# Optimization experiments

Measured on AMD Instinct MI355X. Metric: run time of the kernel, lower is better.

Reference implementation:

```python
import jax, jax.numpy as jnp
import numpy as np

VOCAB = 50257
D_MODEL = 768
N_LAYERS = 4
N_HEADS = 12
D_HEAD = D_MODEL // N_HEADS
MAX_LEN = 5000
EPS = 1e-5


def _make_pe(max_len, d_model):
    # sinusoidal PE, interleaved sin/cos, base n=10000 (matches PositionalEncodingLayer)
    pos = jnp.arange(max_len, dtype=jnp.float32)[:, None]            # [L,1]
    i = jnp.arange(d_model // 2, dtype=jnp.float32)[None, :]         # [1,D/2]
    theta = pos / jnp.power(10000.0, 2.0 * i / d_model)              # [L,D/2]
    pe = jnp.zeros((max_len, d_model), dtype=jnp.float32)
    pe = pe.at[:, 0::2].set(jnp.sin(theta))
    pe = pe.at[:, 1::2].set(jnp.cos(theta))
    return pe


def setup_inputs() -> dict:
    key = jax.random.key(0)
    ks = jax.random.split(key, 10)
    B, S = 2, 1024
    tokens = jax.random.randint(ks[0], (B, S), 0, VOCAB)
    std = 0.02
    embed = jax.random.normal(ks[1], (VOCAB, D_MODEL), jnp.float32) * std
    pe = _make_pe(MAX_LEN, D_MODEL)
    # per-layer stacked params, torch nn.Linear convention: y = x @ W.T + b
    wq_w = jax.random.normal(ks[2], (N_LAYERS, D_MODEL, D_MODEL), jnp.float32) * std
    wk_w = jax.random.normal(ks[3], (N_LAYERS, D_MODEL, D_MODEL), jnp.float32) * std
    wv_w = jax.random.normal(ks[4], (N_LAYERS, D_MODEL, D_MODEL), jnp.float32) * std
    lin_w = jax.random.normal(ks[5], (N_LAYERS, D_MODEL, D_MODEL), jnp.float32) * std
    wq_b = jnp.zeros((N_LAYERS, D_MODEL), jnp.float32)
    wk_b = jnp.zeros((N_LAYERS, D_MODEL), jnp.float32)
    wv_b = jnp.zeros((N_LAYERS, D_MODEL), jnp.float32)
    lin_b = jnp.zeros((N_LAYERS, D_MODEL), jnp.float32)
    n1_s = jnp.ones((N_LAYERS, D_MODEL), jnp.float32)
    n1_b = jnp.zeros((N_LAYERS, D_MODEL), jnp.float32)
    n2_s = jnp.ones((N_LAYERS, D_MODEL), jnp.float32)
    n2_b = jnp.zeros((N_LAYERS, D_MODEL), jnp.float32)
    unembed_w = jax.random.normal(ks[6], (VOCAB, D_MODEL), jnp.float32) * std
    unembed_b = jnp.zeros((VOCAB,), jnp.float32)
    return dict(tokens=tokens, embed=embed, pe=pe,
                wq_w=wq_w, wq_b=wq_b, wk_w=wk_w, wk_b=wk_b, wv_w=wv_w, wv_b=wv_b,
                lin_w=lin_w, lin_b=lin_b, n1_s=n1_s, n1_b=n1_b, n2_s=n2_s, n2_b=n2_b,
                unembed_w=unembed_w, unembed_b=unembed_b)


def _layernorm(x, scale, bias):
    m = jnp.mean(x, axis=-1, keepdims=True)
    v = jnp.mean(jnp.square(x - m), axis=-1, keepdims=True)
    return (x - m) * jax.lax.rsqrt(v + EPS) * scale + bias


def _attn_block(x, wq_w, wq_b, wk_w, wk_b, wv_w, wv_b, lin_w, lin_b, n1_s, n1_b, n2_s, n2_b):
    B, S, D = x.shape
    def proj(w, b):
        y = x @ w.T + b
        return y.reshape(B, S, N_HEADS, D_HEAD).transpose(0, 2, 1, 3)  # [B,H,S,Dh]
    q, k, v = proj(wq_w, wq_b), proj(wk_w, wk_b), proj(wv_w, wv_b)
    scores = jnp.einsum('bhqd,bhkd->bhqk', q, k) / jnp.sqrt(jnp.float32(D_HEAD))
    causal = jnp.tril(jnp.ones((S, S), dtype=bool))
    scores = jnp.where(causal, scores, -jnp.inf)
    probs = jax.nn.softmax(scores, axis=-1)
    attn = jnp.einsum('bhqk,bhkd->bhqd', probs, v)
    attn = attn.transpose(0, 2, 1, 3).reshape(B, S, D)
    x = _layernorm(x + attn, n1_s, n1_b)
    x = _layernorm(x + (x @ lin_w.T + lin_b), n2_s, n2_b)
    return x


def reference(tokens, embed, pe, wq_w, wq_b, wk_w, wk_b, wv_w, wv_b,
              lin_w, lin_b, n1_s, n1_b, n2_s, n2_b, unembed_w, unembed_b):
    B, S = tokens.shape
    x = embed[tokens] + pe[:S]
    for l in range(N_LAYERS):
        x = _attn_block(x, wq_w[l], wq_b[l], wk_w[l], wk_b[l], wv_w[l], wv_b[l],
                        lin_w[l], lin_b[l], n1_s[l], n1_b[l], n2_s[l], n2_b[l])
    logits = x @ unembed_w.T + unembed_b
    return logits
```

## Files before the change

kernel.cpp:

```cpp
#include <hip/hip_runtime.h>
#include <hip/hip_bf16.h>


#define VOCAB 50257
#define DM 768
#define NL 4
#define NH 12
#define DH 64
#define SEQ 1024
#define BATCH 2
#define ROWS (BATCH * SEQ)
#define QKVN (3 * DM)

typedef __attribute__((ext_vector_type(8))) short short8;
typedef __attribute__((ext_vector_type(4))) float f32x4;

__device__ __forceinline__ unsigned short f2bf(float f) {
    union { float f; unsigned u; } v; v.f = f;
    unsigned r = v.u + 0x7FFFu + ((v.u >> 16) & 1u);
    return (unsigned short)(r >> 16);
}

#define GLOAD16(gp, lp)                                                        \
    __builtin_amdgcn_global_load_lds(                                          \
        (const __attribute__((address_space(1))) unsigned int*)(gp),           \
        (__attribute__((address_space(3))) unsigned int*)(lp), 16, 0, 0)

__global__ __launch_bounds__(256) void cvt_kernel(const float* __restrict__ in,
                                                  unsigned short* __restrict__ out,
                                                  int n4) {
    int i = blockIdx.x * 256 + threadIdx.x;
    if (i < n4) {
        float4 v = ((const float4*)in)[i];
        ushort4 o;
        o.x = f2bf(v.x); o.y = f2bf(v.y); o.z = f2bf(v.z); o.w = f2bf(v.w);
        ((ushort4*)out)[i] = o;
    }
}

__global__ __launch_bounds__(256) void cvt_qkv_kernel(const float* __restrict__ wq,
                                                      const float* __restrict__ wk,
                                                      const float* __restrict__ wv,
                                                      unsigned short* __restrict__ dst,
                                                      int n4) {
    int i = blockIdx.x * 256 + threadIdx.x;
    if (i >= n4) return;
    const int PER_L = 3 * DM * DM / 4, PER_W = DM * DM / 4;
    int l = i / PER_L;
    int rem = i - l * PER_L;
    int w = rem / PER_W;
    int r2 = rem - w * PER_W;
    const float* src = (w == 0) ? wq : (w == 1) ? wk : wv;
    float4 v = ((const float4*)src)[(size_t)l * PER_W + r2];
    ushort4 o;
    o.x = f2bf(v.x); o.y = f2bf(v.y); o.z = f2bf(v.z); o.w = f2bf(v.w);
    ((ushort4*)dst)[i] = o;
}

__global__ __launch_bounds__(256) void pack_qkv_bias(const float* __restrict__ bq,
                                                     const float* __restrict__ bk,
                                                     const float* __restrict__ bv,
                                                     float* __restrict__ dst) {
    int i = blockIdx.x * 256 + threadIdx.x;
    if (i >= NL * QKVN) return;
    int l = i / QKVN, c = i - l * QKVN;
    int w = c / DM, cc = c - w * DM;
    const float* src = (w == 0) ? bq : (w == 1) ? bk : bv;
    dst[i] = src[l * DM + cc];
}

__global__ __launch_bounds__(256) void embed_kernel(const int* __restrict__ tok,
                                                    const float* __restrict__ emb,
                                                    const float* __restrict__ pe,
                                                    float* __restrict__ xf,
                                                    unsigned short* __restrict__ xb) {
    int row = blockIdx.x;
    int t = tok[row];
    int s = row & (SEQ - 1);
    #pragma unroll
    for (int j = 0; j < 3; ++j) {
        int c = threadIdx.x + j * 256;
        float v = emb[(size_t)t * DM + c] + pe[(size_t)s * DM + c];
        xf[(size_t)row * DM + c] = v;
        xb[(size_t)row * DM + c] = f2bf(v);
    }
}

__device__ __forceinline__ float block_sum(float x, float* red) {
    #pragma unroll
    for (int off = 32; off > 0; off >>= 1) x += __shfl_down(x, off);
    int w = threadIdx.x >> 6;
    if ((threadIdx.x & 63) == 0) red[w] = x;
    __syncthreads();
    float t = (red[0] + red[1]) + (red[2] + red[3]);
    __syncthreads();
    return t;
}

__global__ __launch_bounds__(256) void ln_kernel(const float* __restrict__ A,
                                                 const float* __restrict__ Bi,
                                                 const float* __restrict__ sc,
                                                 const float* __restrict__ bi,
                                                 float* __restrict__ xf,
                                                 unsigned short* __restrict__ xb) {
    __shared__ float red[4];
    int row = blockIdx.x, tid = threadIdx.x;
    const float* ap = A + (size_t)row * DM;
    const float* bp = Bi + (size_t)row * DM;
    float v[3], sum = 0.f;
    #pragma unroll
    for (int j = 0; j < 3; ++j) { v[j] = ap[tid + j * 256] + bp[tid + j * 256]; sum += v[j]; }
    sum = block_sum(sum, red);
    float mean = sum * (1.f / DM);
    float vs = 0.f;
    #pragma unroll
    for (int j = 0; j < 3; ++j) { float d = v[j] - mean; vs += d * d; }
    vs = block_sum(vs, red);
    float rstd = rsqrtf(vs * (1.f / DM) + 1e-5f);
    #pragma unroll
    for (int j = 0; j < 3; ++j) {
        int c = tid + j * 256;
        float o = (v[j] - mean) * rstd * sc[c] + bi[c];
        xf[(size_t)row * DM + c] = o;
        xb[(size_t)row * DM + c] = f2bf(o);
    }
}

template <int OUT_BF16>
__global__ __launch_bounds__(256) void gemm128(const unsigned short* __restrict__ A,
                                               const unsigned short* __restrict__ B,
                                               const float* __restrict__ bias,
                                               void* __restrict__ C,
                                               int M, int N, int K, int gx) {
    __shared__ __align__(16) unsigned short As[128 * 64];
    __shared__ __align__(16) unsigned short Bs[128 * 64];
    int bid = blockIdx.x;
    const int nwg = gridDim.x;
    if ((nwg & 7) == 0) {
        int q = nwg >> 3;
        bid = (bid & 7) * q + (bid >> 3);
    }
    const int bx = bid % gx, by = bid / gx;
    const int m0 = bx * 128, n0 = by * 128;
    const int tid = threadIdx.x, lane = tid & 63, wid = tid >> 6;
    const int wm = wid >> 1, wn = wid & 1;
    const int lr = lane & 15, lq = lane >> 4;

    const int sr = wid * 32 + (lane >> 3);
    const int sch = lane & 7;
    const int scs = sch ^ (sr & 7);
    const unsigned short* aP[4];
    const unsigned short* bP[4];
    unsigned short* aL[4];
    unsigned short* bL[4];
    #pragma unroll
    for (int i = 0; i < 4; ++i) {
        int r = sr + i * 8;
        aP[i] = A + (size_t)(m0 + r) * K + scs * 8;
        int br = n0 + r; if (br >= N) br = N - 1;
        bP[i] = B + (size_t)br * K + scs * 8;
        aL[i] = &As[r * 64 + sch * 8];
        bL[i] = &Bs[r * 64 + sch * 8];
    }

    f32x4 acc[4][4] = {};

    for (int k0 = 0; k0 < K; k0 += 64) {
        #pragma unroll
        for (int i = 0; i < 4; ++i) GLOAD16(aP[i] + k0, aL[i]);
        #pragma unroll
        for (int i = 0; i < 4; ++i) GLOAD16(bP[i] + k0, bL[i]);
        __syncthreads();
        #pragma unroll
        for (int kk = 0; kk < 2; ++kk) {
            short8 a[4], b[4];
            #pragma unroll
            for (int i = 0; i < 4; ++i) {
                int ar = wm * 64 + i * 16 + lr;
                a[i] = *reinterpret_cast<const short8*>(
                    &As[ar * 64 + (((kk * 4 + lq) ^ (ar & 7)) * 8)]);
                int br = wn * 64 + i * 16 + lr;
                b[i] = *reinterpret_cast<const short8*>(
                    &Bs[br * 64 + (((kk * 4 + lq) ^ (br & 7)) * 8)]);
            }
            #pragma unroll
            for (int i = 0; i < 4; ++i)
                #pragma unroll
                for (int j = 0; j < 4; ++j)
                    acc[i][j] = __builtin_amdgcn_mfma_f32_16x16x32_bf16(a[i], b[j], acc[i][j], 0, 0, 0);
        }
        __syncthreads();
    }
    #pragma unroll
    for (int i = 0; i < 4; ++i) {
        int row = m0 + wm * 64 + i * 16 + lq * 4;
        #pragma unroll
        for (int j = 0; j < 4; ++j) {
            int col = n0 + wn * 64 + j * 16 + lr;
            if (col < N) {
                float bv = bias[col];
                #pragma unroll
                for (int r = 0; r < 4; ++r) {
                    float v = acc[i][j][r] + bv;
                    if (OUT_BF16) ((unsigned short*)C)[(size_t)(row + r) * N + col] = f2bf(v);
                    else          ((float*)C)[(size_t)(row + r) * N + col] = v;
                }
            }
        }
    }
}

__global__ __launch_bounds__(256) void attn_kernel(const unsigned short* __restrict__ Q,
                                                   const unsigned short* __restrict__ K,
                                                   const unsigned short* __restrict__ V,
                                                   int ld,
                                                   float* __restrict__ O) {
    __shared__ __align__(16) unsigned short Ks[64 * 64];
    __shared__ __align__(16) unsigned short Vs[64 * 64];
    __shared__ __align__(16) unsigned short Ps[4][16 * 64];
    const int qb = blockIdx.x;
    const int bh = blockIdx.y;
    const int b = bh / NH, h = bh % NH;
    const int tid = threadIdx.x, lane = tid & 63, w = tid >> 6;
    const int lr = lane & 15, lq = lane >> 4;
    const int wq0 = qb * 64 + w * 16;
    const size_t base = (size_t)b * SEQ * ld + h * DH;
    const size_t obase = (size_t)b * SEQ * DM + h * DH;

    short8 qf[2];
    {
        const unsigned short* qp = Q + base + (size_t)(wq0 + lr) * ld + lq * 8;
        qf[0] = *reinterpret_cast<const short8*>(qp);
        qf[1] = *reinterpret_cast<const short8*>(qp + 32);
    }
    f32x4 o_acc[4] = {};
    float mrow[4], lrow[4];
    #pragma unroll
    for (int r = 0; r < 4; ++r) { mrow[r] = -1e30f; lrow[r] = 0.f; }

    const int srow = tid >> 3, scol = (tid & 7) * 8;
    for (int t = 0; t <= qb; ++t) {
        const int kv0 = t * 64;
        #pragma unroll
        for (int rr = 0; rr < 2; ++rr) {
            int row = rr * 32 + srow;
            {
                const unsigned short* kp = K + base + (size_t)(kv0 + row) * ld + scol;
                short8 v = *reinterpret_cast<const short8*>(kp);
                *reinterpret_cast<short8*>(&Ks[(row * 64 + scol) ^ ((row & 7) << 3)]) = v;
            }
            {
                const unsigned short* vp = V + base + (size_t)(kv0 + row) * ld + scol;
                short8 v = *reinterpret_cast<const short8*>(vp);
                #pragma unroll
                for (int j = 0; j < 8; ++j) {
                    int d = scol + j;
                    Vs[(d * 64 + row) ^ ((d & 7) << 3)] = (unsigned short)v[j];
                }
            }
        }
        __syncthreads();
        if (kv0 <= wq0 + 15) {
            f32x4 s[4];
            #pragma unroll
            for (int n = 0; n < 4; ++n) {
                int br = n * 16 + lr;
                short8 b0 = *reinterpret_cast<const short8*>(&Ks[(br * 64 + lq * 8) ^ ((br & 7) << 3)]);
                short8 b1 = *reinterpret_cast<const short8*>(&Ks[(br * 64 + 32 + lq * 8) ^ ((br & 7) << 3)]);
                f32x4 z = {};
                z = __builtin_amdgcn_mfma_f32_16x16x32_bf16(qf[0], b0, z, 0, 0, 0);
                z = __builtin_amdgcn_mfma_f32_16x16x32_bf16(qf[1], b1, z, 0, 0, 0);
                s[n] = z;
            }
            const bool diag = (t == qb);
            #pragma unroll
            for (int n = 0; n < 4; ++n)
                #pragma unroll
                for (int r = 0; r < 4; ++r) {
                    float v = s[n][r] * 0.125f;
                    if (diag) {
                        int rg = wq0 + lq * 4 + r;
                        int cg = kv0 + n * 16 + lr;
                        if (cg > rg) v = -1e30f;
                    }
                    s[n][r] = v;
                }
            float f[4];
            #pragma unroll
            for (int r = 0; r < 4; ++r) {
                float mx = fmaxf(fmaxf(s[0][r], s[1][r]), fmaxf(s[2][r], s[3][r]));
                #pragma unroll
                for (int off = 1; off < 16; off <<= 1) mx = fmaxf(mx, __shfl_xor(mx, off));
                float mn = fmaxf(mrow[r], mx);
                f[r] = exp2f((mrow[r] - mn) * 1.44269504f);
                mrow[r] = mn;
            }
            #pragma unroll
            for (int n = 0; n < 4; ++n)
                #pragma unroll
                for (int r = 0; r < 4; ++r)
                    s[n][r] = exp2f((s[n][r] - mrow[r]) * 1.44269504f);
            #pragma unroll
            for (int r = 0; r < 4; ++r) {
                float ls = ((s[0][r] + s[1][r]) + (s[2][r] + s[3][r]));
                #pragma unroll
                for (int off = 1; off < 16; off <<= 1) ls += __shfl_xor(ls, off);
                lrow[r] = lrow[r] * f[r] + ls;
            }
            #pragma unroll
            for (int n = 0; n < 4; ++n)
                #pragma unroll
                for (int r = 0; r < 4; ++r) {
                    int pr = lq * 4 + r, pc = n * 16 + lr;
                    Ps[w][(pr * 64 + pc) ^ ((pr & 7) << 3)] = f2bf(s[n][r]);
                }
            #pragma unroll
            for (int n = 0; n < 4; ++n)
                #pragma unroll
                for (int r = 0; r < 4; ++r) o_acc[n][r] *= f[r];
            #pragma unroll
            for (int kk = 0; kk < 2; ++kk) {
                short8 pa = *reinterpret_cast<const short8*>(
                    &Ps[w][(lr * 64 + kk * 32 + lq * 8) ^ ((lr & 7) << 3)]);
                #pragma unroll
                for (int n = 0; n < 4; ++n) {
                    int vr = n * 16 + lr;
                    short8 bv = *reinterpret_cast<const short8*>(
                        &Vs[(vr * 64 + kk * 32 + lq * 8) ^ ((vr & 7) << 3)]);
                    o_acc[n] = __builtin_amdgcn_mfma_f32_16x16x32_bf16(pa, bv, o_acc[n], 0, 0, 0);
                }
            }
        }
        __syncthreads();
    }
    #pragma unroll
    for (int r = 0; r < 4; ++r) {
        float inv = 1.f / lrow[r];
        int row = wq0 + lq * 4 + r;
        #pragma unroll
        for (int n = 0; n < 4; ++n)
            O[obase + (size_t)row * DM + n * 16 + lr] = o_acc[n][r] * inv;
    }
}

extern "C" void kernel_launch(void* const* d_in, const int* in_sizes, int n_in,
                              void* d_out, int out_size, void* d_ws, size_t ws_size,
                              hipStream_t stream) {
    const int*   tokens   = (const int*)d_in[0];
    const float* embed    = (const float*)d_in[1];
    const float* pe       = (const float*)d_in[2];
    const float* wq_w     = (const float*)d_in[3];
    const float* wq_b     = (const float*)d_in[4];
    const float* wk_w     = (const float*)d_in[5];
    const float* wk_b     = (const float*)d_in[6];
    const float* wv_w     = (const float*)d_in[7];
    const float* wv_b     = (const float*)d_in[8];
    const float* lin_w    = (const float*)d_in[9];
    const float* lin_b    = (const float*)d_in[10];
    const float* n1_s     = (const float*)d_in[11];
    const float* n1_b     = (const float*)d_in[12];
    const float* n2_s     = (const float*)d_in[13];
    const float* n2_b     = (const float*)d_in[14];
    const float* unemb_w  = (const float*)d_in[15];
    const float* unemb_b  = (const float*)d_in[16];

    char* ws = (char*)d_ws;
    size_t off = 0;
    auto carve = [&](size_t bytes) { char* p = ws + off; off += (bytes + 255) & ~(size_t)255; return p; };
    float*          xf     = (float*)carve((size_t)ROWS * DM * 4);
    float*          yb     = (float*)carve((size_t)ROWS * DM * 4);
    unsigned short* xb     = (unsigned short*)carve((size_t)ROWS * DM * 2);
    unsigned short* qkv    = (unsigned short*)carve((size_t)ROWS * QKVN * 2);
    unsigned short* wqkv_h = (unsigned short*)carve((size_t)NL * QKVN * DM * 2);
    unsigned short* lin_h  = (unsigned short*)carve((size_t)NL * DM * DM * 2);
    unsigned short* ue_h   = (unsigned short*)carve((size_t)VOCAB * DM * 2);
    float*          qkvb   = (float*)carve((size_t)NL * QKVN * 4);

    {
        int nq4 = NL * QKVN * DM / 4;
        cvt_qkv_kernel<<<(nq4 + 255) / 256, 256, 0, stream>>>(wq_w, wk_w, wv_w, wqkv_h, nq4);
        int nl4 = NL * DM * DM / 4;
        cvt_kernel<<<(nl4 + 255) / 256, 256, 0, stream>>>(lin_w, lin_h, nl4);
        int nu4 = VOCAB * DM / 4;
        cvt_kernel<<<(nu4 + 255) / 256, 256, 0, stream>>>(unemb_w, ue_h, nu4);
        pack_qkv_bias<<<(NL * QKVN + 255) / 256, 256, 0, stream>>>(wq_b, wk_b, wv_b, qkvb);
    }
    embed_kernel<<<ROWS, 256, 0, stream>>>(tokens, embed, pe, xf, xb);

    const int gx = ROWS / 128;
    for (int l = 0; l < NL; ++l) {
        gemm128<1><<<gx * (QKVN / 128), 256, 0, stream>>>(
            xb, wqkv_h + (size_t)l * QKVN * DM, qkvb + l * QKVN, qkv,
            ROWS, QKVN, DM, gx);
        attn_kernel<<<dim3(SEQ / 64, BATCH * NH), 256, 0, stream>>>(
            qkv, qkv + DM, qkv + 2 * DM, QKVN, yb);
        ln_kernel<<<ROWS, 256, 0, stream>>>(xf, yb, n1_s + l * DM, n1_b + l * DM, xf, xb);
        gemm128<0><<<gx * (DM / 128), 256, 0, stream>>>(
            xb, lin_h + (size_t)l * DM * DM, lin_b + l * DM, yb,
            ROWS, DM, DM, gx);
        ln_kernel<<<ROWS, 256, 0, stream>>>(xf, yb, n2_s + l * DM, n2_b + l * DM, xf, xb);
    }
    const int gyu = (VOCAB + 127) / 128;
    gemm128<0><<<gx * gyu, 256, 0, stream>>>(
        xb, ue_h, unemb_b, (float*)d_out, ROWS, VOCAB, DM, gx);
}
```

Before: 809.3 us.

## Use panel-resident B GEMM for unembedding and wave-per-row layernorm

```diff
diff --git a/kernel.cpp b/kernel.cpp
--- a/kernel.cpp
+++ b/kernel.cpp
@@ -25,6 +25,8 @@
     __builtin_amdgcn_global_load_lds(                                          \
         (const __attribute__((address_space(1))) unsigned int*)(gp),           \
         (__attribute__((address_space(3))) unsigned int*)(lp), 16, 0, 0)
+
+#define VMCNT0()  asm volatile("s_waitcnt vmcnt(0)" ::: "memory")
 
 __global__ __launch_bounds__(256) void cvt_kernel(const float* __restrict__ in,
                                                   unsigned short* __restrict__ out,
@@ -86,43 +88,53 @@
     }
 }
 
-__device__ __forceinline__ float block_sum(float x, float* red) {
-    #pragma unroll
-    for (int off = 32; off > 0; off >>= 1) x += __shfl_down(x, off);
-    int w = threadIdx.x >> 6;
-    if ((threadIdx.x & 63) == 0) red[w] = x;
-    __syncthreads();
-    float t = (red[0] + red[1]) + (red[2] + red[3]);
-    __syncthreads();
-    return t;
-}
-
 __global__ __launch_bounds__(256) void ln_kernel(const float* __restrict__ A,
                                                  const float* __restrict__ Bi,
                                                  const float* __restrict__ sc,
                                                  const float* __restrict__ bi,
                                                  float* __restrict__ xf,
                                                  unsigned short* __restrict__ xb) {
-    __shared__ float red[4];
-    int row = blockIdx.x, tid = threadIdx.x;
+    const int w = threadIdx.x >> 6, lane = threadIdx.x & 63;
+    const int row = blockIdx.x * 4 + w;
     const float* ap = A + (size_t)row * DM;
     const float* bp = Bi + (size_t)row * DM;
-    float v[3], sum = 0.f;
-    #pragma unroll
-    for (int j = 0; j < 3; ++j) { v[j] = ap[tid + j * 256] + bp[tid + j * 256]; sum += v[j]; }
-    sum = block_sum(sum, red);
+    float4 v[3];
+    float sum = 0.f;
+    #pragma unroll
+    for (int j = 0; j < 3; ++j) {
+        int c4 = lane * 3 + j;
+        float4 a4 = ((const float4*)ap)[c4];
+        float4 b4 = ((const float4*)bp)[c4];
+        v[j].x = a4.x + b4.x; v[j].y = a4.y + b4.y;
+        v[j].z = a4.z + b4.z; v[j].w = a4.w + b4.w;
+        sum += (v[j].x + v[j].y) + (v[j].z + v[j].w);
+    }
+    #pragma unroll
+    for (int off = 32; off > 0; off >>= 1) sum += __shfl_xor(sum, off);
     float mean = sum * (1.f / DM);
     float vs = 0.f;
     #pragma unroll
-    for (int j = 0; j < 3; ++j) { float d = v[j] - mean; vs += d * d; }
-    vs = block_sum(vs, red);
+    for (int j = 0; j < 3; ++j) {
+        float dx = v[j].x - mean, dy = v[j].y - mean, dz = v[j].z - mean, dw = v[j].w - mean;
+        vs += dx * dx + dy * dy + dz * dz + dw * dw;
+    }
+    #pragma unroll
+    for (int off = 32; off > 0; off >>= 1) vs += __shfl_xor(vs, off);
     float rstd = rsqrtf(vs * (1.f / DM) + 1e-5f);
     #pragma unroll
     for (int j = 0; j < 3; ++j) {
-        int c = tid + j * 256;
-        float o = (v[j] - mean) * rstd * sc[c] + bi[c];
-        xf[(size_t)row * DM + c] = o;
-        xb[(size_t)row * DM + c] = f2bf(o);
+        int c4 = lane * 3 + j;
+        float4 s4 = ((const float4*)sc)[c4];
+        float4 b4 = ((const float4*)bi)[c4];
+        float4 o;
+        o.x = (v[j].x - mean) * rstd * s4.x + b4.x;
+        o.y = (v[j].y - mean) * rstd * s4.y + b4.y;
+        o.z = (v[j].z - mean) * rstd * s4.z + b4.z;
+        o.w = (v[j].w - mean) * rstd * s4.w + b4.w;
+        ((float4*)(xf + (size_t)row * DM))[c4] = o;
+        ushort4 h;
+        h.x = f2bf(o.x); h.y = f2bf(o.y); h.z = f2bf(o.z); h.w = f2bf(o.w);
+        ((ushort4*)(xb + (size_t)row * DM))[c4] = h;
     }
 }
 
@@ -204,6 +216,98 @@
                     float v = acc[i][j][r] + bv;
                     if (OUT_BF16) ((unsigned short*)C)[(size_t)(row + r) * N + col] = f2bf(v);
                     else          ((float*)C)[(size_t)(row + r) * N + col] = v;
+                }
+            }
+        }
+    }
+}
+
+__global__ __launch_bounds__(512, 4) void gemm_bpanel(const unsigned short* __restrict__ A,
+                                                      const unsigned short* __restrict__ B,
+                                                      const float* __restrict__ bias,
+                                                      float* __restrict__ C,
+                                                      int N) {
+    constexpr int PANEL = 48;
+    constexpr int KD = DM;
+    constexpr int NCH = KD / 8;
+    __shared__ __align__(16) unsigned short Bs[PANEL * KD];
+    const int n0 = blockIdx.x * PANEL;
+    const int tid = threadIdx.x, lane = tid & 63, w = tid >> 6;
+    const int lr = lane & 15, lq = lane >> 4;
+
+    #pragma unroll
+    for (int i = 0; i < 9; ++i) {
+        int l = tid + i * 512;
+        int row = l / NCH, c = l - row * NCH;
+        int brow = n0 + row; if (brow >= N) brow = N - 1;
+        int cs = (c & ~7) | ((c ^ row) & 7);
+        GLOAD16(B + (size_t)brow * KD + cs * 8, &Bs[l * 8]);
+    }
+    VMCNT0();
+    __syncthreads();
+
+    float bv[3];
+    #pragma unroll
+    for (int j = 0; j < 3; ++j) {
+        int col = n0 + j * 16 + lr;
+        bv[j] = bias[col < N ? col : N - 1];
+    }
+
+    for (int mt = 0; mt < 4; ++mt) {
+        const int m0 = (w + mt * 8) * 64;
+        const unsigned short* aR[4];
+        #pragma unroll
+        for (int f = 0; f < 4; ++f)
+            aR[f] = A + (size_t)(m0 + f * 16 + lr) * KD + lq * 8;
+        f32x4 acc[4][3] = {};
+        short8 aE[4], aO[4];
+        #pragma unroll
+        for (int f = 0; f < 4; ++f)
+            aE[f] = *reinterpret_cast<const short8*>(aR[f]);
+        for (int kt = 0; kt < 24; kt += 2) {
+            #pragma unroll
+            for (int f = 0; f < 4; ++f)
+                aO[f] = *reinterpret_cast<const short8*>(aR[f] + (kt + 1) * 32);
+            short8 b0[3];
+            #pragma unroll
+            for (int j = 0; j < 3; ++j) {
+                int c = kt * 4 + lq, row = j * 16 + lr;
+                b0[j] = *reinterpret_cast<const short8*>(
+                    &Bs[row * KD + (((c & ~7) | ((c ^ row) & 7)) * 8)]);
+            }
+            #pragma unroll
+            for (int f = 0; f < 4; ++f)
+                #pragma unroll
+                for (int j = 0; j < 3; ++j)
+                    acc[f][j] = __builtin_amdgcn_mfma_f32_16x16x32_bf16(aE[f], b0[j], acc[f][j], 0, 0, 0);
+            if (kt + 2 < 24) {
+                #pragma unroll
+                for (int f = 0; f < 4; ++f)
+                    aE[f] = *reinterpret_cast<const short8*>(aR[f] + (kt + 2) * 32);
+            }
+            short8 b1[3];
+            #pragma unroll
+            for (int j = 0; j < 3; ++j) {
+                int c = (kt + 1) * 4 + lq, row = j * 16 + lr;
+                b1[j] = *reinterpret_cast<const short8*>(
+                    &Bs[row * KD + (((c & ~7) | ((c ^ row) & 7)) * 8)]);
+            }
+            #pragma unroll
+            for (int f = 0; f < 4; ++f)
+                #pragma unroll
+                for (int j = 0; j < 3; ++j)
+                    acc[f][j] = __builtin_amdgcn_mfma_f32_16x16x32_bf16(aO[f], b1[j], acc[f][j], 0, 0, 0);
+        }
+        #pragma unroll
+        for (int f = 0; f < 4; ++f) {
+            int rowb = m0 + f * 16 + lq * 4;
+            #pragma unroll
+            for (int j = 0; j < 3; ++j) {
+                int col = n0 + j * 16 + lr;
+                if (col < N) {
+                    #pragma unroll
+                    for (int r = 0; r < 4; ++r)
+                        C[(size_t)(rowb + r) * N + col] = acc[f][j][r] + bv[j];
                 }
             }
         }
@@ -394,13 +498,13 @@
             ROWS, QKVN, DM, gx);
         attn_kernel<<<dim3(SEQ / 64, BATCH * NH), 256, 0, stream>>>(
             qkv, qkv + DM, qkv + 2 * DM, QKVN, yb);
-        ln_kernel<<<ROWS, 256, 0, stream>>>(xf, yb, n1_s + l * DM, n1_b + l * DM, xf, xb);
+        ln_kernel<<<ROWS / 4, 256, 0, stream>>>(xf, yb, n1_s + l * DM, n1_b + l * DM, xf, xb);
         gemm128<0><<<gx * (DM / 128), 256, 0, stream>>>(
             xb, lin_h + (size_t)l * DM * DM, lin_b + l * DM, yb,
             ROWS, DM, DM, gx);
-        ln_kernel<<<ROWS, 256, 0, stream>>>(xf, yb, n2_s + l * DM, n2_b + l * DM, xf, xb);
-    }
-    const int gyu = (VOCAB + 127) / 128;
-    gemm128<0><<<gx * gyu, 256, 0, stream>>>(
-        xb, ue_h, unemb_b, (float*)d_out, ROWS, VOCAB, DM, gx);
-}
+        ln_kernel<<<ROWS / 4, 256, 0, stream>>>(xf, yb, n2_s + l * DM, n2_b + l * DM, xf, xb);
+    }
+    const int npanels = (VOCAB + 47) / 48;
+    gemm_bpanel<<<npanels, 512, 0, stream>>>(
+        xb, ue_h, unemb_b, (float*)d_out, VOCAB);
+}
```

After: 1.937 ms. 139% more time.
